# Performance work log

Hardware: AMD Instinct MI355X
Metric: run time of the kernel (lower is better)

## Reference

```python
import jax, jax.numpy as jnp
import numpy as np

N_NODES = 50000
N_EDGES = 1_600_000
IN_DIM = 128
HID = 64


def gcn_conv(x, src, dst, w, W, b, n):
    # PyG GCNConv(normalize=True, add_self_loops=True):
    # add self loops with weight 1, sym-normalize, x@W (no bias in lin), scatter-add, +bias
    loop = jnp.arange(n)
    s = jnp.concatenate([src, loop])
    d = jnp.concatenate([dst, loop])
    ww = jnp.concatenate([w, jnp.ones((n,), w.dtype)])
    deg = jax.ops.segment_sum(ww, d, num_segments=n)                 # [n]
    dis = jnp.where(deg > 0, jax.lax.rsqrt(deg), 0.0)                # deg^{-1/2}, inf->0
    norm = dis[s] * ww * dis[d]                                      # [E+n]
    h = x @ W                                                        # [n, out]
    msg = h[s] * norm[:, None]                                       # gather + scale
    out = jax.ops.segment_sum(msg, d, num_segments=n)                # scatter-add at dst
    return out + b


def setup_inputs() -> dict:
    key = jax.random.key(0)
    ks = jax.random.split(key, 9)
    X = jax.random.normal(ks[0], (N_NODES, IN_DIM), dtype=jnp.float32)
    edge_index = jax.random.randint(ks[1], (2, N_EDGES), 0, N_NODES, dtype=jnp.int64)
    edge_weight = jax.random.uniform(ks[2], (N_EDGES,), dtype=jnp.float32)
    s1 = 1.0 / np.sqrt(IN_DIM)
    s2 = 1.0 / np.sqrt(HID)
    W1 = jax.random.uniform(ks[3], (IN_DIM, HID), jnp.float32, -s1, s1)
    b1 = jax.random.uniform(ks[4], (HID,), jnp.float32, -s1, s1)
    W2 = jax.random.uniform(ks[5], (HID, HID), jnp.float32, -s2, s2)
    b2 = jax.random.uniform(ks[6], (HID,), jnp.float32, -s2, s2)
    Wl = jax.random.uniform(ks[7], (HID, 1), jnp.float32, -s2, s2)
    bl = jax.random.uniform(ks[8], (1,), jnp.float32, -s2, s2)
    return {"X": X, "edge_index": edge_index, "edge_weight": edge_weight,
            "W1": W1, "b1": b1, "W2": W2, "b2": b2, "Wl": Wl, "bl": bl}


def reference(X, edge_index, edge_weight, W1, b1, W2, b2, Wl, bl):
    n = X.shape[0]
    src, dst = edge_index[0], edge_index[1]
    h = jax.nn.relu(gcn_conv(X, src, dst, edge_weight, W1, b1, n))
    # F.dropout(p=0.2) is identity in eval mode
    h = jax.nn.relu(gcn_conv(h, src, dst, edge_weight, W2, b2, n))
    return jax.nn.sigmoid(h @ Wl + bl).squeeze(1)   # [n]
```

## Files before the change

### kernel.cpp

```cpp
#include <hip/hip_runtime.h>

typedef float f32x2 __attribute__((ext_vector_type(2)));

#define A2B 512
#define A2T 512
#define STG 3200

__device__ __forceinline__ long ld_idx(const void* idx, long pos, int is64) {
  return is64 ? (long)((const long long*)idx)[pos]
              : (long)((const int*)idx)[pos];
}

__device__ __forceinline__ int detect_is64(const void* idx) {
  const unsigned long long* p = (const unsigned long long*)idx;
  unsigned long long v = p[threadIdx.x & 63];
  return (__ballot((v >> 32) != 0ull) == 0ull) ? 1 : 0;
}

__device__ __forceinline__ uint4 pack16_fp8(const float* acc) {
  uint4 o;
  unsigned v;
  v = 0;
  v = __builtin_amdgcn_cvt_pk_fp8_f32(acc[0],  acc[1],  v, false);
  v = __builtin_amdgcn_cvt_pk_fp8_f32(acc[2],  acc[3],  v, true);
  o.x = v; v = 0;
  v = __builtin_amdgcn_cvt_pk_fp8_f32(acc[4],  acc[5],  v, false);
  v = __builtin_amdgcn_cvt_pk_fp8_f32(acc[6],  acc[7],  v, true);
  o.y = v; v = 0;
  v = __builtin_amdgcn_cvt_pk_fp8_f32(acc[8],  acc[9],  v, false);
  v = __builtin_amdgcn_cvt_pk_fp8_f32(acc[10], acc[11], v, true);
  o.z = v; v = 0;
  v = __builtin_amdgcn_cvt_pk_fp8_f32(acc[12], acc[13], v, false);
  v = __builtin_amdgcn_cvt_pk_fp8_f32(acc[14], acc[15], v, true);
  o.w = v;
  return o;
}

__global__ __launch_bounds__(256) void k_front(const void* __restrict__ idx,
                                               unsigned* __restrict__ histT,
                                               long E, int chunk, unsigned M,
                                               const float* __restrict__ X,
                                               const float* __restrict__ W1,
                                               unsigned char* __restrict__ h, int n) {
  __shared__ float smem[2048];
  const int t = threadIdx.x;
  if (blockIdx.x < A2B) {
    unsigned* cnt = (unsigned*)smem;
    const int b = blockIdx.x;
    const int is64 = detect_is64(idx);
    cnt[t] = 0;
    __syncthreads();
    const long e0 = (long)b * chunk;
    long e1 = e0 + chunk; if (e1 > E) e1 = E;
    for (long e = e0 + t; e < e1; e += 256) {
      unsigned d = (unsigned)ld_idx(idx, E + e, is64);
      atomicAdd(&cnt[__umulhi(d, M)], 1u);
    }
    __syncthreads();
    histT[(size_t)t * A2B + b] = cnt[t];
    return;
  }
  float* Ws = smem;
  for (int i = t; i < 2048; i += 256)
    ((float4*)Ws)[i] = ((const float4*)W1)[i];
  __syncthreads();
  int gid = (blockIdx.x - A2B) * 256 + t;
  int node = gid >> 2;
  int fg = (gid & 3) * 16;
  if (node >= n) return;
  const float4* xr4 = (const float4*)(X + (size_t)node * 128);
  float acc[16];
#pragma unroll
  for (int f = 0; f < 16; ++f) acc[f] = 0.0f;
  for (int k4 = 0; k4 < 32; ++k4) {
    float4 x = xr4[k4];
#pragma unroll
    for (int kk = 0; kk < 4; ++kk) {
      float xv = (kk == 0) ? x.x : (kk == 1) ? x.y : (kk == 2) ? x.z : x.w;
      const float4* wrow = (const float4*)(Ws + (k4 * 4 + kk) * 64 + fg);
#pragma unroll
      for (int f4 = 0; f4 < 4; ++f4) {
        float4 w = wrow[f4];
        acc[f4 * 4 + 0] = fmaf(xv, w.x, acc[f4 * 4 + 0]);
        acc[f4 * 4 + 1] = fmaf(xv, w.y, acc[f4 * 4 + 1]);
        acc[f4 * 4 + 2] = fmaf(xv, w.z, acc[f4 * 4 + 2]);
        acc[f4 * 4 + 3] = fmaf(xv, w.w, acc[f4 * 4 + 3]);
      }
    }
  }
  *(uint4*)(h + (size_t)node * 64 + fg) = pack16_fp8(acc);
}

__global__ __launch_bounds__(256) void k_colscan(const unsigned* __restrict__ histT,
                                                 unsigned* __restrict__ baseT,
                                                 unsigned* __restrict__ colsum) {
  __shared__ unsigned sh[256];
  const int k = blockIdx.x, t = threadIdx.x;
  const uint2 v = ((const uint2*)(histT + (size_t)k * A2B))[t];
  unsigned s = v.x + v.y;
  sh[t] = s;
  __syncthreads();
  for (int off = 1; off < 256; off <<= 1) {
    unsigned u = (t >= off) ? sh[t - off] : 0;
    __syncthreads();
    sh[t] += u;
    __syncthreads();
  }
  unsigned excl = sh[t] - s;
  uint2 o; o.x = excl; o.y = excl + v.x;
  ((uint2*)(baseT + (size_t)k * A2B))[t] = o;
  if (t == 255) colsum[k] = sh[255];
}

__global__ __launch_bounds__(A2T) void k_bucket(const void* __restrict__ idx,
                                                const float* __restrict__ w,
                                                const unsigned* __restrict__ baseT,
                                                const unsigned* __restrict__ colsum,
                                                uint2* __restrict__ recs,
                                                long E, int chunk, unsigned M) {
  __shared__ uint2 stage[STG];
  __shared__ unsigned cnt[256], lofs[256], lbase[256], bcol[256], scanb[256];
  const int b = blockIdx.x, t = threadIdx.x;
  const long e0 = (long)b * chunk;
  long e1 = e0 + chunk; if (e1 > E) e1 = E;
  const int m = (int)(e1 - e0);
  const int is64 = detect_is64(idx);
  if (t < 256) scanb[t] = colsum[t];
  __syncthreads();
  for (int off = 1; off < 256; off <<= 1) {
    unsigned u = 0;
    if (t < 256 && t >= off) u = scanb[t - off];
    __syncthreads();
    if (t < 256) scanb[t] += u;
    __syncthreads();
  }
  if (t < 256) {
    bcol[t] = (scanb[t] - colsum[t]) + baseT[(size_t)t * A2B + b];
    cnt[t] = 0;
  }
  __syncthreads();
  unsigned short dc[8]; unsigned char kc[8];
  int nk = 0;
  for (long e = e0 + t; e < e1; e += A2T, ++nk) {
    unsigned d = (unsigned)ld_idx(idx, E + e, is64);
    unsigned kb = __umulhi(d, M);
    dc[nk] = (unsigned short)d; kc[nk] = (unsigned char)kb;
    atomicAdd(&cnt[kb], 1u);
  }
  __syncthreads();
  if (t < 256) scanb[t] = cnt[t];
  __syncthreads();
  for (int off = 1; off < 256; off <<= 1) {
    unsigned u = 0;
    if (t < 256 && t >= off) u = scanb[t - off];
    __syncthreads();
    if (t < 256) scanb[t] += u;
    __syncthreads();
  }
  if (t < 256) { unsigned ex = scanb[t] - cnt[t]; lbase[t] = ex; lofs[t] = ex; }
  __syncthreads();
  nk = 0;
  for (long e = e0 + t; e < e1; e += A2T, ++nk) {
    unsigned s = (unsigned)ld_idx(idx, e, is64);
    float wv = w[e];
    unsigned kb = kc[nk];
    unsigned pos = atomicAdd(&lofs[kb], 1u);
    stage[pos] = make_uint2(s | ((unsigned)dc[nk] << 16), __float_as_uint(wv));
  }
  __syncthreads();
  for (int i = t; i < m; i += A2T) {
    uint2 r = stage[i];
    unsigned kb = __umulhi(r.x >> 16, M);
    recs[bcol[kb] + (unsigned)i - lbase[kb]] = r;
  }
}

__global__ __launch_bounds__(1024) void k_build(const uint2* __restrict__ recs,
                                                const unsigned* __restrict__ colsum,
                                                int* __restrict__ rowptr,
                                                float* __restrict__ dis,
                                                float2* __restrict__ edges,
                                                int n, int dwidth, long E) {
  __shared__ float wsum[256];
  __shared__ unsigned cnt[256], lofs[256], scanb[256];
  __shared__ int shr0, shr1;
  const int k = blockIdx.x, t = threadIdx.x;
  const int d0 = k * dwidth;
  if (t < 256) scanb[t] = colsum[t];
  __syncthreads();
  for (int off = 1; off < 256; off <<= 1) {
    unsigned u = 0;
    if (t < 256 && t >= off) u = scanb[t - off];
    __syncthreads();
    if (t < 256) scanb[t] += u;
    __syncthreads();
  }
  if (t == k) { shr1 = (int)scanb[t]; shr0 = (int)(scanb[t] - colsum[t]); }
  if (t < 256) { wsum[t] = 0.0f; cnt[t] = 0; }
  __syncthreads();
  const int r0 = shr0, r1 = shr1;
  const int m = r1 - r0;
  for (int i = t; i < m; i += 1024) {
    uint2 r = recs[r0 + i];
    int dl = (int)(r.x >> 16) - d0;
    atomicAdd(&cnt[dl], 1u);
    atomicAdd(&wsum[dl], __uint_as_float(r.y));
  }
  __syncthreads();
  if (t < 256) scanb[t] = cnt[t];
  __syncthreads();
  for (int off = 1; off < 256; off <<= 1) {
    unsigned u = 0;
    if (t < 256 && t >= off) u = scanb[t - off];
    __syncthreads();
    if (t < 256) scanb[t] += u;
    __syncthreads();
  }
  if (t < 256) {
    unsigned ex = scanb[t] - cnt[t];
    lofs[t] = (unsigned)r0 + ex;
    int d = d0 + t;
    if (t < dwidth && d < n) {
      rowptr[d] = r0 + (int)ex;
      dis[d] = rsqrtf(1.0f + wsum[t]);
    }
  }
  if (k == gridDim.x - 1 && t == 0) rowptr[n] = (int)E;
  __syncthreads();
  for (int i = t; i < m; i += 1024) {
    uint2 r = recs[r0 + i];
    unsigned pos = atomicAdd(&lofs[(int)(r.x >> 16) - d0], 1u);
    edges[pos] = make_float2(__uint_as_float(r.x & 0xffffu), __uint_as_float(r.y));
  }
}

__global__ __launch_bounds__(256) void k_norm(float2* __restrict__ edges,
                                              const float* __restrict__ dis, long E) {
  long i0 = (long)blockIdx.x * 256 + threadIdx.x;
  long stride = (long)gridDim.x * 256;
  for (long i = i0; i < E; i += stride) {
    float2 r = edges[i];
    r.y *= dis[__float_as_int(r.x)];
    edges[i] = r;
  }
}

__device__ __forceinline__ void gather_acc(const unsigned char* __restrict__ h,
                                           const float2* __restrict__ edges,
                                           int beg, int end, int eg, int fl,
                                           float* acc) {
  f32x2 a0 = {0.0f, 0.0f}, a1 = {0.0f, 0.0f}, a2 = {0.0f, 0.0f}, a3 = {0.0f, 0.0f};
  const unsigned char* hf = h + fl * 8;
  for (int base = beg; base < end; base += 32) {
    float2 rv[8];
#pragma unroll
    for (int s = 0; s < 8; ++s) {
      int idx = base + s * 4 + eg;
      rv[s] = edges[min(idx, end - 1)];
    }
    uint2 hv[8];
#pragma unroll
    for (int s = 0; s < 8; ++s)
      hv[s] = *(const uint2*)(hf + (size_t)__float_as_int(rv[s].x) * 64);
#pragma unroll
    for (int s = 0; s < 8; ++s) {
      float w = (base + s * 4 + eg < end) ? rv[s].y : 0.0f;
      f32x2 nj2 = {w, w};
      a0 += __builtin_amdgcn_cvt_pk_f32_fp8(hv[s].x, false) * nj2;
      a1 += __builtin_amdgcn_cvt_pk_f32_fp8(hv[s].x, true)  * nj2;
      a2 += __builtin_amdgcn_cvt_pk_f32_fp8(hv[s].y, false) * nj2;
      a3 += __builtin_amdgcn_cvt_pk_f32_fp8(hv[s].y, true)  * nj2;
    }
  }
  acc[0] = a0[0]; acc[1] = a0[1]; acc[2] = a1[0]; acc[3] = a1[1];
  acc[4] = a2[0]; acc[5] = a2[1]; acc[6] = a3[0]; acc[7] = a3[1];
#pragma unroll
  for (int off = 8; off < 32; off <<= 1)
#pragma unroll
    for (int i = 0; i < 8; ++i) acc[i] += __shfl_xor(acc[i], off);
}

__device__ __forceinline__ void add_bias_self(const unsigned char* __restrict__ h,
                                              const float* __restrict__ b,
                                              int node, int fl, float s0, float* acc) {
  uint2 hv = *(const uint2*)(h + (size_t)node * 64 + fl * 8);
  f32x2 q0 = __builtin_amdgcn_cvt_pk_f32_fp8(hv.x, false);
  f32x2 q1 = __builtin_amdgcn_cvt_pk_f32_fp8(hv.x, true);
  f32x2 q2 = __builtin_amdgcn_cvt_pk_f32_fp8(hv.y, false);
  f32x2 q3 = __builtin_amdgcn_cvt_pk_f32_fp8(hv.y, true);
  float hs[8] = {q0[0], q0[1], q1[0], q1[1], q2[0], q2[1], q3[0], q3[1]};
  float4 bv0 = *(const float4*)(b + fl * 8);
  float4 bv1 = *(const float4*)(b + fl * 8 + 4);
  float bb[8] = {bv0.x, bv0.y, bv0.z, bv0.w, bv1.x, bv1.y, bv1.z, bv1.w};
  float s2 = s0 * s0;
#pragma unroll
  for (int i = 0; i < 8; ++i) acc[i] += bb[i] + hs[i] * s2;
}

__global__ __launch_bounds__(256) void k_gather_mid(const unsigned char* __restrict__ h,
                                                    const float* __restrict__ dis,
                                                    const float2* __restrict__ edges,
                                                    const int* __restrict__ rowptr,
                                                    const float* __restrict__ b1,
                                                    const float* __restrict__ W2,
                                                    unsigned char* __restrict__ h2, int n) {
  __shared__ float W2s[64 * 64];
  __shared__ float xs[8 * 64];
  const int t = threadIdx.x;
  for (int i = t; i < 1024; i += 256)
    ((float4*)W2s)[i] = ((const float4*)W2)[i];
  int lane = t & 63;
  int l32 = lane & 31;
  int fl = lane & 7;
  int eg = (lane >> 3) & 3;
  int nl = t >> 5;
  int node = blockIdx.x * 8 + nl;
  int beg = 0, end = 0; float s0 = 0.0f;
  if (node < n) { beg = rowptr[node]; end = rowptr[node + 1]; s0 = dis[node]; }
  float acc[8];
  gather_acc(h, edges, beg, end, eg, fl, acc);
  if (node < n) {
#pragma unroll
    for (int i = 0; i < 8; ++i) acc[i] *= s0;
    add_bias_self(h, b1, node, fl, s0, acc);
    if (eg == 0) {
#pragma unroll
      for (int i = 0; i < 8; ++i) xs[nl * 64 + fl * 8 + i] = fmaxf(acc[i], 0.0f);
    }
  }
  __syncthreads();
  int tl = l32;
  int node2 = blockIdx.x * 8 + (t >> 5);
  if (node2 >= n) return;
  const float* xrow = xs + (t >> 5) * 64;
  int f = tl * 2;
  float a0 = 0.0f, a1 = 0.0f;
#pragma unroll 8
  for (int k = 0; k < 64; ++k) {
    float xk = xrow[k];
    f32x2 wv = *(const f32x2*)(W2s + k * 64 + f);
    a0 = fmaf(xk, wv[0], a0);
    a1 = fmaf(xk, wv[1], a1);
  }
  unsigned v = __builtin_amdgcn_cvt_pk_fp8_f32(a0, a1, 0u, false);
  *(unsigned short*)(h2 + (size_t)node2 * 64 + f) = (unsigned short)v;
}

__global__ __launch_bounds__(256) void k_gather_fin(const unsigned char* __restrict__ h,
                                                    const float* __restrict__ dis,
                                                    const float2* __restrict__ edges,
                                                    const int* __restrict__ rowptr,
                                                    const float* __restrict__ b2,
                                                    const float* __restrict__ Wl,
                                                    const float* __restrict__ bl,
                                                    float* __restrict__ out, int n) {
  int lane = threadIdx.x & 63;
  int l32 = lane & 31;
  int fl = lane & 7;
  int eg = (lane >> 3) & 3;
  int node = blockIdx.x * 8 + (int)(threadIdx.x >> 5);
  if (node >= n) return;
  int beg = rowptr[node], end = rowptr[node + 1];
  float s0 = dis[node];
  float acc[8];
  gather_acc(h, edges, beg, end, eg, fl, acc);
#pragma unroll
  for (int i = 0; i < 8; ++i) acc[i] *= s0;
  add_bias_self(h, b2, node, fl, s0, acc);
  float4 wl0 = *(const float4*)(Wl + fl * 8);
  float4 wl1 = *(const float4*)(Wl + fl * 8 + 4);
  float wl[8] = {wl0.x, wl0.y, wl0.z, wl0.w, wl1.x, wl1.y, wl1.z, wl1.w};
  float v = 0.0f;
#pragma unroll
  for (int i = 0; i < 8; ++i) v += fmaxf(acc[i], 0.0f) * wl[i];
#pragma unroll
  for (int off = 1; off < 8; off <<= 1) v += __shfl_xor(v, off);
  if (l32 == 0) out[node] = 1.0f / (1.0f + expf(-(v + bl[0])));
}

extern "C" void kernel_launch(void* const* d_in, const int* in_sizes, int n_in,
                              void* d_out, int out_size, void* d_ws, size_t ws_size,
                              hipStream_t stream) {
  const float* X  = (const float*)d_in[0];
  const void*  EI = d_in[1];
  const float* EW = (const float*)d_in[2];
  const float* W1 = (const float*)d_in[3];
  const float* b1 = (const float*)d_in[4];
  const float* W2 = (const float*)d_in[5];
  const float* b2 = (const float*)d_in[6];
  const float* Wl = (const float*)d_in[7];
  const float* bl = (const float*)d_in[8];
  float* out = (float*)d_out;

  const int  n = in_sizes[0] / 128;
  const long E = (long)in_sizes[1] / 2;

  const int chunk  = (int)((E + A2B - 1) / A2B);
  const int dwidth = (n + 255) / 256;
  const unsigned M = (unsigned)((0x100000000ULL + (unsigned)dwidth - 1) / (unsigned)dwidth);

  auto align = [](size_t x) { return (x + 255) & ~(size_t)255; };
  char* ws = (char*)d_ws;
  size_t off = 0;
  float*         dis    = (float*)(ws + off);         off += align((size_t)n * 4);
  int*           rowptr = (int*)(ws + off);           off += align((size_t)(n + 1) * 4);
  unsigned*      colsum = (unsigned*)(ws + off);      off += align(256 * 4);
  unsigned*      histT  = (unsigned*)(ws + off);      off += align((size_t)A2B * 256 * 4);
  unsigned*      baseT  = (unsigned*)(ws + off);      off += align((size_t)A2B * 256 * 4);
  uint2*         recs   = (uint2*)(ws + off);         off += align((size_t)E * 8);
  float2*        edges  = (float2*)(ws + off);        off += align((size_t)E * 8);
  unsigned char* A      = (unsigned char*)(ws + off); off += align((size_t)n * 64);
  unsigned char* A2     = (unsigned char*)(ws + off); off += align((size_t)n * 64);

  const int nbW = (n + 7) / 8;
  const int nbG = (n * 4 + 255) / 256;
  const int nbN = 2048;

  k_front<<<A2B + nbG, dim3(256), 0, stream>>>(EI, histT, E, chunk, M, X, W1, A, n);
  k_colscan<<<256, 256, 0, stream>>>(histT, baseT, colsum);
  k_bucket<<<A2B, A2T, 0, stream>>>(EI, EW, baseT, colsum, recs, E, chunk, M);
  k_build<<<256, 1024, 0, stream>>>(recs, colsum, rowptr, dis, edges, n, dwidth, E);
  k_norm<<<nbN, dim3(256), 0, stream>>>(edges, dis, E);

  k_gather_mid<<<nbW, dim3(256), 0, stream>>>(A, dis, edges, rowptr, b1, W2, A2, n);
  k_gather_fin<<<nbW, dim3(256), 0, stream>>>(A2, dis, edges, rowptr, b2, Wl, bl, out, n);
}
```

Measured before the change: 218.7 us.

## Split edge placement into its own kernel fused with source-norm scaling; widen gather batch

The CSR build is split so k_build only computes counts, rowptr and dis. A new k_place kernel scatters records into CSR order and multiplies each weight by dis[src] as it writes, which removes the separate k_norm pass that re-read and re-wrote every edge. Splitting is needed because dis must be complete grid-wide before any edge can be scaled. The cost is re-reading recs and redoing the colsum scan in a second launch. The gather loop also batches 12 edges per iteration instead of 8 for more memory-level parallelism, at the cost of more registers and more masked loads on short rows.

Result: faster. 211.2 us (-3.4%).

```diff
diff --git a/kernel.cpp b/kernel.cpp
--- a/kernel.cpp
+++ b/kernel.cpp
@@ -179,10 +179,9 @@
                                                 const unsigned* __restrict__ colsum,
                                                 int* __restrict__ rowptr,
                                                 float* __restrict__ dis,
-                                                float2* __restrict__ edges,
                                                 int n, int dwidth, long E) {
   __shared__ float wsum[256];
-  __shared__ unsigned cnt[256], lofs[256], scanb[256];
+  __shared__ unsigned cnt[256], scanb[256];
   __shared__ int shr0, shr1;
   const int k = blockIdx.x, t = threadIdx.x;
   const int d0 = k * dwidth;
@@ -218,7 +217,6 @@
   }
   if (t < 256) {
     unsigned ex = scanb[t] - cnt[t];
-    lofs[t] = (unsigned)r0 + ex;
     int d = d0 + t;
     if (t < dwidth && d < n) {
       rowptr[d] = r0 + (int)ex;
@@ -226,22 +224,41 @@
     }
   }
   if (k == gridDim.x - 1 && t == 0) rowptr[n] = (int)E;
-  __syncthreads();
+}
+
+__global__ __launch_bounds__(1024) void k_place(const uint2* __restrict__ recs,
+                                                const unsigned* __restrict__ colsum,
+                                                const int* __restrict__ rowptr,
+                                                const float* __restrict__ dis,
+                                                float2* __restrict__ edges,
+                                                int n, int dwidth) {
+  __shared__ unsigned lofs[256], scanb[256];
+  __shared__ int shr0, shr1;
+  const int k = blockIdx.x, t = threadIdx.x;
+  const int d0 = k * dwidth;
+  if (t < 256) scanb[t] = colsum[t];
+  __syncthreads();
+  for (int off = 1; off < 256; off <<= 1) {
+    unsigned u = 0;
+    if (t < 256 && t >= off) u = scanb[t - off];
+    __syncthreads();
+    if (t < 256) scanb[t] += u;
+    __syncthreads();
+  }
+  if (t == k) { shr1 = (int)scanb[t]; shr0 = (int)(scanb[t] - colsum[t]); }
+  if (t < 256) {
+    int d = d0 + t;
+    lofs[t] = (t < dwidth && d < n) ? (unsigned)rowptr[d] : 0u;
+  }
+  __syncthreads();
+  const int r0 = shr0, r1 = shr1;
+  const int m = r1 - r0;
   for (int i = t; i < m; i += 1024) {
     uint2 r = recs[r0 + i];
+    unsigned src = r.x & 0xffffu;
+    float wn = __uint_as_float(r.y) * dis[src];
     unsigned pos = atomicAdd(&lofs[(int)(r.x >> 16) - d0], 1u);
-    edges[pos] = make_float2(__uint_as_float(r.x & 0xffffu), __uint_as_float(r.y));
-  }
-}
-
-__global__ __launch_bounds__(256) void k_norm(float2* __restrict__ edges,
-                                              const float* __restrict__ dis, long E) {
-  long i0 = (long)blockIdx.x * 256 + threadIdx.x;
-  long stride = (long)gridDim.x * 256;
-  for (long i = i0; i < E; i += stride) {
-    float2 r = edges[i];
-    r.y *= dis[__float_as_int(r.x)];
-    edges[i] = r;
+    edges[pos] = make_float2(__uint_as_float(src), wn);
   }
 }
 
@@ -251,19 +268,19 @@
                                            float* acc) {
   f32x2 a0 = {0.0f, 0.0f}, a1 = {0.0f, 0.0f}, a2 = {0.0f, 0.0f}, a3 = {0.0f, 0.0f};
   const unsigned char* hf = h + fl * 8;
-  for (int base = beg; base < end; base += 32) {
-    float2 rv[8];
-#pragma unroll
-    for (int s = 0; s < 8; ++s) {
+  for (int base = beg; base < end; base += 48) {
+    float2 rv[12];
+#pragma unroll
+    for (int s = 0; s < 12; ++s) {
       int idx = base + s * 4 + eg;
       rv[s] = edges[min(idx, end - 1)];
     }
-    uint2 hv[8];
-#pragma unroll
-    for (int s = 0; s < 8; ++s)
+    uint2 hv[12];
+#pragma unroll
+    for (int s = 0; s < 12; ++s)
       hv[s] = *(const uint2*)(hf + (size_t)__float_as_int(rv[s].x) * 64);
 #pragma unroll
-    for (int s = 0; s < 8; ++s) {
+    for (int s = 0; s < 12; ++s) {
       float w = (base + s * 4 + eg < end) ? rv[s].y : 0.0f;
       f32x2 nj2 = {w, w};
       a0 += __builtin_amdgcn_cvt_pk_f32_fp8(hv[s].x, false) * nj2;
@@ -414,13 +431,12 @@
 
   const int nbW = (n + 7) / 8;
   const int nbG = (n * 4 + 255) / 256;
-  const int nbN = 2048;
 
   k_front<<<A2B + nbG, dim3(256), 0, stream>>>(EI, histT, E, chunk, M, X, W1, A, n);
   k_colscan<<<256, 256, 0, stream>>>(histT, baseT, colsum);
   k_bucket<<<A2B, A2T, 0, stream>>>(EI, EW, baseT, colsum, recs, E, chunk, M);
-  k_build<<<256, 1024, 0, stream>>>(recs, colsum, rowptr, dis, edges, n, dwidth, E);
-  k_norm<<<nbN, dim3(256), 0, stream>>>(edges, dis, E);
+  k_build<<<256, 1024, 0, stream>>>(recs, colsum, rowptr, dis, n, dwidth, E);
+  k_place<<<256, 1024, 0, stream>>>(recs, colsum, rowptr, dis, edges, n, dwidth);
 
   k_gather_mid<<<nbW, dim3(256), 0, stream>>>(A, dis, edges, rowptr, b1, W2, A2, n);
   k_gather_fin<<<nbW, dim3(256), 0, stream>>>(A2, dis, edges, rowptr, b2, Wl, bl, out, n);
```

## Replace two-level bucket sort CSR build with global-atomic counting sort

Applied to the files above, without the earlier changes.

Replaces the histogram/colscan/bucket/build/norm pipeline with a direct counting sort: per-node degree and weight sums via global atomics, a single-block scan producing rowptr, dis and per-node offsets, then an atomic scatter of edges folding in the source normalization. This removes the staged intermediate record buffer and two kernel launches. It trades them for heavy global atomic contention, a serial one-block scan, and uncoalesced scatter writes. Edge order within each row becomes nondeterministic. The gather loop also widens its batch from 8 to 12 edges per iteration for more memory parallelism.

After: 545.9 us. 150% more time.

```diff
diff --git a/kernel.cpp b/kernel.cpp
--- a/kernel.cpp
+++ b/kernel.cpp
@@ -2,9 +2,9 @@
 
 typedef float f32x2 __attribute__((ext_vector_type(2)));
 
-#define A2B 512
-#define A2T 512
-#define STG 3200
+
+#define NBD 512
+#define NBS 1024
 
 __device__ __forceinline__ long ld_idx(const void* idx, long pos, int is64) {
   return is64 ? (long)((const long long*)idx)[pos]
@@ -37,34 +37,30 @@
 }
 
 __global__ __launch_bounds__(256) void k_front(const void* __restrict__ idx,
-                                               unsigned* __restrict__ histT,
-                                               long E, int chunk, unsigned M,
+                                               const float* __restrict__ w,
+                                               uint2* __restrict__ degw, long E,
                                                const float* __restrict__ X,
                                                const float* __restrict__ W1,
                                                unsigned char* __restrict__ h, int n) {
   __shared__ float smem[2048];
   const int t = threadIdx.x;
-  if (blockIdx.x < A2B) {
-    unsigned* cnt = (unsigned*)smem;
-    const int b = blockIdx.x;
+  if (blockIdx.x < NBD) {
     const int is64 = detect_is64(idx);
-    cnt[t] = 0;
-    __syncthreads();
-    const long e0 = (long)b * chunk;
-    long e1 = e0 + chunk; if (e1 > E) e1 = E;
-    for (long e = e0 + t; e < e1; e += 256) {
+    long i0 = (long)blockIdx.x * 256 + t;
+    long stride = (long)NBD * 256;
+    for (long e = i0; e < E; e += stride) {
       unsigned d = (unsigned)ld_idx(idx, E + e, is64);
-      atomicAdd(&cnt[__umulhi(d, M)], 1u);
-    }
-    __syncthreads();
-    histT[(size_t)t * A2B + b] = cnt[t];
+      float wv = w[e];
+      atomicAdd(&degw[d].x, 1u);
+      atomicAdd((float*)&degw[d].y, wv);
+    }
     return;
   }
   float* Ws = smem;
   for (int i = t; i < 2048; i += 256)
     ((float4*)Ws)[i] = ((const float4*)W1)[i];
   __syncthreads();
-  int gid = (blockIdx.x - A2B) * 256 + t;
+  int gid = (blockIdx.x - NBD) * 256 + t;
   int node = gid >> 2;
   int fg = (gid & 3) * 16;
   if (node >= n) return;
@@ -80,168 +76,61 @@
       const float4* wrow = (const float4*)(Ws + (k4 * 4 + kk) * 64 + fg);
 #pragma unroll
       for (int f4 = 0; f4 < 4; ++f4) {
-        float4 w = wrow[f4];
-        acc[f4 * 4 + 0] = fmaf(xv, w.x, acc[f4 * 4 + 0]);
-        acc[f4 * 4 + 1] = fmaf(xv, w.y, acc[f4 * 4 + 1]);
-        acc[f4 * 4 + 2] = fmaf(xv, w.z, acc[f4 * 4 + 2]);
-        acc[f4 * 4 + 3] = fmaf(xv, w.w, acc[f4 * 4 + 3]);
+        float4 w4 = wrow[f4];
+        acc[f4 * 4 + 0] = fmaf(xv, w4.x, acc[f4 * 4 + 0]);
+        acc[f4 * 4 + 1] = fmaf(xv, w4.y, acc[f4 * 4 + 1]);
+        acc[f4 * 4 + 2] = fmaf(xv, w4.z, acc[f4 * 4 + 2]);
+        acc[f4 * 4 + 3] = fmaf(xv, w4.w, acc[f4 * 4 + 3]);
       }
     }
   }
   *(uint4*)(h + (size_t)node * 64 + fg) = pack16_fp8(acc);
 }
 
-__global__ __launch_bounds__(256) void k_colscan(const unsigned* __restrict__ histT,
-                                                 unsigned* __restrict__ baseT,
-                                                 unsigned* __restrict__ colsum) {
-  __shared__ unsigned sh[256];
-  const int k = blockIdx.x, t = threadIdx.x;
-  const uint2 v = ((const uint2*)(histT + (size_t)k * A2B))[t];
-  unsigned s = v.x + v.y;
+__global__ __launch_bounds__(1024) void k_scan(const uint2* __restrict__ degw,
+                                               int* __restrict__ rowptr,
+                                               unsigned* __restrict__ lofs,
+                                               float* __restrict__ dis, int n, long E) {
+  __shared__ unsigned sh[1024];
+  const int t = threadIdx.x;
+  const int per = (n + 1023) >> 10;
+  const int i0 = t * per;
+  const int i1 = min(i0 + per, n);
+  unsigned s = 0;
+  for (int i = i0; i < i1; ++i) s += degw[i].x;
   sh[t] = s;
   __syncthreads();
-  for (int off = 1; off < 256; off <<= 1) {
+  for (int off = 1; off < 1024; off <<= 1) {
     unsigned u = (t >= off) ? sh[t - off] : 0;
     __syncthreads();
     sh[t] += u;
     __syncthreads();
   }
-  unsigned excl = sh[t] - s;
-  uint2 o; o.x = excl; o.y = excl + v.x;
-  ((uint2*)(baseT + (size_t)k * A2B))[t] = o;
-  if (t == 255) colsum[k] = sh[255];
-}
-
-__global__ __launch_bounds__(A2T) void k_bucket(const void* __restrict__ idx,
-                                                const float* __restrict__ w,
-                                                const unsigned* __restrict__ baseT,
-                                                const unsigned* __restrict__ colsum,
-                                                uint2* __restrict__ recs,
-                                                long E, int chunk, unsigned M) {
-  __shared__ uint2 stage[STG];
-  __shared__ unsigned cnt[256], lofs[256], lbase[256], bcol[256], scanb[256];
-  const int b = blockIdx.x, t = threadIdx.x;
-  const long e0 = (long)b * chunk;
-  long e1 = e0 + chunk; if (e1 > E) e1 = E;
-  const int m = (int)(e1 - e0);
+  unsigned run = sh[t] - s;
+  for (int i = i0; i < i1; ++i) {
+    uint2 dw = degw[i];
+    rowptr[i] = (int)run;
+    lofs[i] = run;
+    dis[i] = rsqrtf(1.0f + __uint_as_float(dw.y));
+    run += dw.x;
+  }
+  if (t == 0) rowptr[n] = (int)E;
+}
+
+__global__ __launch_bounds__(256) void k_scatter(const void* __restrict__ idx,
+                                                 const float* __restrict__ w,
+                                                 const float* __restrict__ dis,
+                                                 unsigned* __restrict__ lofs,
+                                                 float2* __restrict__ edges, long E) {
   const int is64 = detect_is64(idx);
-  if (t < 256) scanb[t] = colsum[t];
-  __syncthreads();
-  for (int off = 1; off < 256; off <<= 1) {
-    unsigned u = 0;
-    if (t < 256 && t >= off) u = scanb[t - off];
-    __syncthreads();
-    if (t < 256) scanb[t] += u;
-    __syncthreads();
-  }
-  if (t < 256) {
-    bcol[t] = (scanb[t] - colsum[t]) + baseT[(size_t)t * A2B + b];
-    cnt[t] = 0;
-  }
-  __syncthreads();
-  unsigned short dc[8]; unsigned char kc[8];
-  int nk = 0;
-  for (long e = e0 + t; e < e1; e += A2T, ++nk) {
-    unsigned d = (unsigned)ld_idx(idx, E + e, is64);
-    unsigned kb = __umulhi(d, M);
-    dc[nk] = (unsigned short)d; kc[nk] = (unsigned char)kb;
-    atomicAdd(&cnt[kb], 1u);
-  }
-  __syncthreads();
-  if (t < 256) scanb[t] = cnt[t];
-  __syncthreads();
-  for (int off = 1; off < 256; off <<= 1) {
-    unsigned u = 0;
-    if (t < 256 && t >= off) u = scanb[t - off];
-    __syncthreads();
-    if (t < 256) scanb[t] += u;
-    __syncthreads();
-  }
-  if (t < 256) { unsigned ex = scanb[t] - cnt[t]; lbase[t] = ex; lofs[t] = ex; }
-  __syncthreads();
-  nk = 0;
-  for (long e = e0 + t; e < e1; e += A2T, ++nk) {
-    unsigned s = (unsigned)ld_idx(idx, e, is64);
-    float wv = w[e];
-    unsigned kb = kc[nk];
-    unsigned pos = atomicAdd(&lofs[kb], 1u);
-    stage[pos] = make_uint2(s | ((unsigned)dc[nk] << 16), __float_as_uint(wv));
-  }
-  __syncthreads();
-  for (int i = t; i < m; i += A2T) {
-    uint2 r = stage[i];
-    unsigned kb = __umulhi(r.x >> 16, M);
-    recs[bcol[kb] + (unsigned)i - lbase[kb]] = r;
-  }
-}
-
-__global__ __launch_bounds__(1024) void k_build(const uint2* __restrict__ recs,
-                                                const unsigned* __restrict__ colsum,
-                                                int* __restrict__ rowptr,
-                                                float* __restrict__ dis,
-                                                float2* __restrict__ edges,
-                                                int n, int dwidth, long E) {
-  __shared__ float wsum[256];
-  __shared__ unsigned cnt[256], lofs[256], scanb[256];
-  __shared__ int shr0, shr1;
-  const int k = blockIdx.x, t = threadIdx.x;
-  const int d0 = k * dwidth;
-  if (t < 256) scanb[t] = colsum[t];
-  __syncthreads();
-  for (int off = 1; off < 256; off <<= 1) {
-    unsigned u = 0;
-    if (t < 256 && t >= off) u = scanb[t - off];
-    __syncthreads();
-    if (t < 256) scanb[t] += u;
-    __syncthreads();
-  }
-  if (t == k) { shr1 = (int)scanb[t]; shr0 = (int)(scanb[t] - colsum[t]); }
-  if (t < 256) { wsum[t] = 0.0f; cnt[t] = 0; }
-  __syncthreads();
-  const int r0 = shr0, r1 = shr1;
-  const int m = r1 - r0;
-  for (int i = t; i < m; i += 1024) {
-    uint2 r = recs[r0 + i];
-    int dl = (int)(r.x >> 16) - d0;
-    atomicAdd(&cnt[dl], 1u);
-    atomicAdd(&wsum[dl], __uint_as_float(r.y));
-  }
-  __syncthreads();
-  if (t < 256) scanb[t] = cnt[t];
-  __syncthreads();
-  for (int off = 1; off < 256; off <<= 1) {
-    unsigned u = 0;
-    if (t < 256 && t >= off) u = scanb[t - off];
-    __syncthreads();
-    if (t < 256) scanb[t] += u;
-    __syncthreads();
-  }
-  if (t < 256) {
-    unsigned ex = scanb[t] - cnt[t];
-    lofs[t] = (unsigned)r0 + ex;
-    int d = d0 + t;
-    if (t < dwidth && d < n) {
-      rowptr[d] = r0 + (int)ex;
-      dis[d] = rsqrtf(1.0f + wsum[t]);
-    }
-  }
-  if (k == gridDim.x - 1 && t == 0) rowptr[n] = (int)E;
-  __syncthreads();
-  for (int i = t; i < m; i += 1024) {
-    uint2 r = recs[r0 + i];
-    unsigned pos = atomicAdd(&lofs[(int)(r.x >> 16) - d0], 1u);
-    edges[pos] = make_float2(__uint_as_float(r.x & 0xffffu), __uint_as_float(r.y));
-  }
-}
-
-__global__ __launch_bounds__(256) void k_norm(float2* __restrict__ edges,
-                                              const float* __restrict__ dis, long E) {
   long i0 = (long)blockIdx.x * 256 + threadIdx.x;
   long stride = (long)gridDim.x * 256;
-  for (long i = i0; i < E; i += stride) {
-    float2 r = edges[i];
-    r.y *= dis[__float_as_int(r.x)];
-    edges[i] = r;
+  for (long e = i0; e < E; e += stride) {
+    unsigned s = (unsigned)ld_idx(idx, e, is64);
+    unsigned d = (unsigned)ld_idx(idx, E + e, is64);
+    float wn = w[e] * dis[s];
+    unsigned pos = atomicAdd(&lofs[d], 1u);
+    edges[pos] = make_float2(__uint_as_float(s), wn);
   }
 }
 
@@ -251,19 +140,19 @@
                                            float* acc) {
   f32x2 a0 = {0.0f, 0.0f}, a1 = {0.0f, 0.0f}, a2 = {0.0f, 0.0f}, a3 = {0.0f, 0.0f};
   const unsigned char* hf = h + fl * 8;
-  for (int base = beg; base < end; base += 32) {
-    float2 rv[8];
-#pragma unroll
-    for (int s = 0; s < 8; ++s) {
+  for (int base = beg; base < end; base += 48) {
+    float2 rv[12];
+#pragma unroll
+    for (int s = 0; s < 12; ++s) {
       int idx = base + s * 4 + eg;
       rv[s] = edges[min(idx, end - 1)];
     }
-    uint2 hv[8];
-#pragma unroll
-    for (int s = 0; s < 8; ++s)
+    uint2 hv[12];
+#pragma unroll
+    for (int s = 0; s < 12; ++s)
       hv[s] = *(const uint2*)(hf + (size_t)__float_as_int(rv[s].x) * 64);
 #pragma unroll
-    for (int s = 0; s < 8; ++s) {
+    for (int s = 0; s < 12; ++s) {
       float w = (base + s * 4 + eg < end) ? rv[s].y : 0.0f;
       f32x2 nj2 = {w, w};
       a0 += __builtin_amdgcn_cvt_pk_f32_fp8(hv[s].x, false) * nj2;
@@ -395,32 +284,25 @@
   const int  n = in_sizes[0] / 128;
   const long E = (long)in_sizes[1] / 2;
 
-  const int chunk  = (int)((E + A2B - 1) / A2B);
-  const int dwidth = (n + 255) / 256;
-  const unsigned M = (unsigned)((0x100000000ULL + (unsigned)dwidth - 1) / (unsigned)dwidth);
-
   auto align = [](size_t x) { return (x + 255) & ~(size_t)255; };
   char* ws = (char*)d_ws;
   size_t off = 0;
   float*         dis    = (float*)(ws + off);         off += align((size_t)n * 4);
   int*           rowptr = (int*)(ws + off);           off += align((size_t)(n + 1) * 4);
-  unsigned*      colsum = (unsigned*)(ws + off);      off += align(256 * 4);
-  unsigned*      histT  = (unsigned*)(ws + off);      off += align((size_t)A2B * 256 * 4);
-  unsigned*      baseT  = (unsigned*)(ws + off);      off += align((size_t)A2B * 256 * 4);
-  uint2*         recs   = (uint2*)(ws + off);         off += align((size_t)E * 8);
+  uint2*         degw   = (uint2*)(ws + off);         off += align((size_t)n * 8);
+  unsigned*      lofs   = (unsigned*)(ws + off);      off += align((size_t)n * 4);
   float2*        edges  = (float2*)(ws + off);        off += align((size_t)E * 8);
   unsigned char* A      = (unsigned char*)(ws + off); off += align((size_t)n * 64);
   unsigned char* A2     = (unsigned char*)(ws + off); off += align((size_t)n * 64);
 
   const int nbW = (n + 7) / 8;
   const int nbG = (n * 4 + 255) / 256;
-  const int nbN = 2048;
-
-  k_front<<<A2B + nbG, dim3(256), 0, stream>>>(EI, histT, E, chunk, M, X, W1, A, n);
-  k_colscan<<<256, 256, 0, stream>>>(histT, baseT, colsum);
-  k_bucket<<<A2B, A2T, 0, stream>>>(EI, EW, baseT, colsum, recs, E, chunk, M);
-  k_build<<<256, 1024, 0, stream>>>(recs, colsum, rowptr, dis, edges, n, dwidth, E);
-  k_norm<<<nbN, dim3(256), 0, stream>>>(edges, dis, E);
+
+  hipMemsetAsync(degw, 0, (size_t)n * 8, stream);
+
+  k_front<<<NBD + nbG, dim3(256), 0, stream>>>(EI, EW, degw, E, X, W1, A, n);
+  k_scan<<<1, dim3(1024), 0, stream>>>(degw, rowptr, lofs, dis, n, E);
+  k_scatter<<<NBS, dim3(256), 0, stream>>>(EI, EW, dis, lofs, edges, E);
 
   k_gather_mid<<<nbW, dim3(256), 0, stream>>>(A, dis, edges, rowptr, b1, W2, A2, n);
   k_gather_fin<<<nbW, dim3(256), 0, stream>>>(A2, dis, edges, rowptr, b2, Wl, bl, out, n);
```
